# Performance work log

Hardware: AMD Instinct MI355X
Metric: run time of the kernel (lower is better)

The kernel has to match this reference:

```python
import jax, jax.numpy as jnp
import numpy as np

N_NODES = 10000
N_EDGES = 640000
HIDDEN = 128
N_LAYERS = 3
DECAY_RATE = 1.0


def setup_inputs() -> dict:
    key = jax.random.key(0)
    ks = jax.random.split(key, 16)
    D, L = HIDDEN, N_LAYERS
    s = 1.0 / np.sqrt(D)
    inp = {
        "x": jax.random.normal(ks[0], (N_NODES, D), dtype=jnp.float32),
        "edge_index": jax.random.randint(ks[1], (2, N_EDGES), 0, N_NODES, dtype=jnp.int32),
        "confidences": jax.random.uniform(ks[2], (N_NODES,), dtype=jnp.float32),
        # per-layer message MLP params, stacked over layers: [L, D, D] / [L, D]
        "msg_W1": jax.random.normal(ks[3], (L, D, D), dtype=jnp.float32) * s,
        "msg_b1": jnp.zeros((L, D), dtype=jnp.float32),
        "msg_W2": jax.random.normal(ks[4], (L, D, D), dtype=jnp.float32) * s,
        "msg_b2": jnp.zeros((L, D), dtype=jnp.float32),
        # per-layer self MLP params
        "self_W1": jax.random.normal(ks[5], (L, D, D), dtype=jnp.float32) * s,
        "self_b1": jnp.zeros((L, D), dtype=jnp.float32),
        "self_W2": jax.random.normal(ks[6], (L, D, D), dtype=jnp.float32) * s,
        "self_b2": jnp.zeros((L, D), dtype=jnp.float32),
        # layer-importance score net: Linear(D,D) -> ReLU -> Linear(D,1)
        "score_W1": jax.random.normal(ks[7], (D, D), dtype=jnp.float32) * s,
        "score_b1": jnp.zeros((D,), dtype=jnp.float32),
        "score_W2": jax.random.normal(ks[8], (D, 1), dtype=jnp.float32) * s,
        "score_b2": jnp.zeros((1,), dtype=jnp.float32),
    }
    return inp


def _mlp2(h, W1, b1, W2, b2):
    return jax.nn.relu(h @ W1 + b1) @ W2 + b2


def reference(x, edge_index, confidences,
              msg_W1, msg_b1, msg_W2, msg_b2,
              self_W1, self_b1, self_W2, self_b2,
              score_W1, score_b1, score_W2, score_b2):
    src, dst = edge_index[0], edge_index[1]
    # confidence-weighted edge weights: exp(-decay * |c_src - c_dst|)
    edge_weights = jnp.exp(-DECAY_RATE * jnp.abs(confidences[src] - confidences[dst]))  # [E]

    h = x
    layer_outputs = []
    for i in range(N_LAYERS):
        messages = _mlp2(h[src], msg_W1[i], msg_b1[i], msg_W2[i], msg_b2[i])  # [E, D]
        messages = messages * edge_weights[:, None]
        aggr = jax.ops.segment_sum(messages, dst, num_segments=N_NODES)  # [N, D]
        self_loop = _mlp2(h, self_W1[i], self_b1[i], self_W2[i], self_b2[i])
        h = jax.nn.relu(aggr + self_loop)  # dropout is identity in eval mode
        layer_outputs.append(h)

    stacked = jnp.stack(layer_outputs, axis=0)  # [L, N, D]
    scores = _mlp2(stacked, score_W1, score_b1, score_W2, score_b2)[..., 0]  # [L, N]
    layer_weights = jax.nn.softmax(scores, axis=0)  # softmax over layers
    output = jnp.sum(layer_weights[:, :, None] * stacked, axis=0)  # [N, D]
    return output, stacked, layer_weights
```

## Files before the change

kernel.cpp:

```cpp
#include <hip/hip_runtime.h>

#define NN 10000
#define NE 640000
#define D 128
#define NF (NN * D)
#define WS 136
#define WBYTES (D * WS * 2)
#define WCHUNKS (WBYTES / 1024)
#define NBLK 100
#define EPB (NE / NBLK)
#define MPAD 1000000
#define NIT 4
#define GBP 79
#define NCS ((NN + 127) / 128)
#define MZB ((MPAD / 2 + 1023) / 1024)

typedef __bf16 bf16x8 __attribute__((ext_vector_type(8)));
typedef __bf16 bf16x2 __attribute__((ext_vector_type(2)));
typedef float f32x4 __attribute__((ext_vector_type(4)));

__device__ __forceinline__ void async_copy16(const void* g, void* l) {
    __builtin_amdgcn_global_load_lds(
        (const __attribute__((address_space(1))) unsigned int*)g,
        (__attribute__((address_space(3))) unsigned int*)l, 16, 0, 0);
}


__global__ __launch_bounds__(256) void hist_prep_kernel(
    const int* __restrict__ ei, int* __restrict__ cnt_blk, int* __restrict__ local_rank,
    const float2* __restrict__ x2, bf16x2* __restrict__ xbf,
    const float* __restrict__ mW1, const float* __restrict__ mW2,
    const float* __restrict__ sW1, const float* __restrict__ sW2,
    const float* __restrict__ scW1, __bf16* __restrict__ wt,
    float4* __restrict__ metaz) {
    __shared__ unsigned int hist[NN / 2];
    int b = blockIdx.x, t = threadIdx.x;
    if (b < NBLK) {
        for (int i = t; i < NN / 2; i += 256) hist[i] = 0u;
        __syncthreads();
        int base = b * EPB;
#pragma unroll 1
        for (int i = 0; i < EPB / 256; i++) {
            int e = base + i * 256 + t;
            int d = ei[NE + e];
            int sh = (d & 1) * 16;
            unsigned int old = atomicAdd(&hist[d >> 1], 1u << sh);
            local_rank[e] = (old >> sh) & 0xFFFFu;
        }
        __syncthreads();
        for (int i = t; i < NN; i += 256)
            cnt_blk[b * NN + i] = (hist[i >> 1] >> ((i & 1) * 16)) & 0xFFFFu;
    } else if (b < NBLK + 2500) {
        int i = (b - NBLK) * 256 + t;
        float2 v = x2[i];
        bf16x2 o;
        o.x = (__bf16)v.x;
        o.y = (__bf16)v.y;
        xbf[i] = o;
    } else if (b < NBLK + 2513) {
        int m = b - (NBLK + 2500);
        const float* W = (m < 3)   ? mW1 + (size_t)m * D * D
                       : (m < 6)   ? mW2 + (size_t)(m - 3) * D * D
                       : (m < 9)   ? sW1 + (size_t)(m - 6) * D * D
                       : (m < 12)  ? sW2 + (size_t)(m - 9) * D * D
                                   : scW1;
        __bf16* o = wt + (size_t)m * D * WS;
        for (int i = t; i < D * D; i += 256) {
            int k = i >> 7, n = i & 127;
            o[n * WS + k] = (__bf16)W[i];
        }
    } else {
        int base = (b - (NBLK + 2513)) * 1024 + t;
#pragma unroll
        for (int i = 0; i < 4; i++) {
            int idx = base + i * 256;
            if (idx < MPAD / 2) metaz[idx] = make_float4(0.f, 0.f, 0.f, 0.f);
        }
    }
}

__global__ void scan_kernel(const int* __restrict__ cnt, int* __restrict__ row_ptr) {
    __shared__ int lds[256];
    int t = threadIdx.x;
    const int CH = (NN + 255) / 256;
    int base = t * CH;
    int s = 0;
    for (int i = 0; i < CH; i++) {
        int idx = base + i;
        if (idx < NN) s += (cnt[idx] + 31) & ~31;
    }
    lds[t] = s;
    __syncthreads();
    for (int off = 1; off < 256; off <<= 1) {
        int v = (t >= off) ? lds[t - off] : 0;
        __syncthreads();
        lds[t] += v;
        __syncthreads();
    }
    int run = (t == 0) ? 0 : lds[t - 1];
    for (int i = 0; i < CH; i++) {
        int idx = base + i;
        if (idx < NN) {
            row_ptr[idx] = run;
            run += (cnt[idx] + 31) & ~31;
        }
    }
    if (t == 255) row_ptr[NN] = lds[255];
}

__global__ void scatter_kernel(const int* __restrict__ ei, const float* __restrict__ conf,
                               const int* __restrict__ local_rank,
                               const int* __restrict__ cnt_blk,
                               const int* __restrict__ row_ptr, float2* __restrict__ meta) {
    int e = blockIdx.x * 256 + threadIdx.x;
    if (e >= NE) return;
    int s = ei[e];
    int d = ei[NE + e];
    int blk = e / EPB;
    int pos = row_ptr[d] + cnt_blk[blk * NN + d] + local_rank[e];
    meta[pos] = make_float2(__int_as_float(s), expf(-fabsf(conf[s] - conf[d])));
}


__device__ __forceinline__ void mlp_tiles_body(
    const __bf16* __restrict__ Abf,
    const __bf16* __restrict__ Wt1, const float* __restrict__ b1,
    const __bf16* __restrict__ Wt2, const float* __restrict__ b2,
    __bf16* __restrict__ Mbf, float* __restrict__ Cself, int write_bf,
    __bf16 (*Wl)[D * WS], __bf16 (*Tl)[16 * WS], int bx, int t) {
    int wid = t >> 6, lane = t & 63;
    int m16 = lane & 15, q = lane >> 4;

    for (int c = wid; c < 2 * WCHUNKS; c += 2) {
        const char* src = (c < WCHUNKS) ? (const char*)Wt1 + c * 1024
                                        : (const char*)Wt2 + (c - WCHUNKS) * 1024;
        async_copy16(src + lane * 16, (char*)&Wl[0][0] + c * 1024 + lane * 16);
    }

    int rowb = bx * (NIT * 32) + wid * 16;

    bf16x8 af[4];
    {
        int arow = min(rowb + m16, NN - 1);
#pragma unroll
        for (int kk = 0; kk < 4; kk++)
            af[kk] = *(const bf16x8*)&Abf[(size_t)arow * D + kk * 32 + q * 8];
    }
    float b1v[8], b2v[8];
#pragma unroll
    for (int ct = 0; ct < 8; ct++) { b1v[ct] = b1[ct * 16 + m16]; b2v[ct] = b2[ct * 16 + m16]; }

    __syncthreads();

#pragma unroll
    for (int it = 0; it < NIT; it++) {
        int row0 = rowb + it * 32;
        bf16x8 afn[4];
        if (it + 1 < NIT) {
            int arown = min(row0 + 32 + m16, NN - 1);
#pragma unroll
            for (int kk = 0; kk < 4; kk++)
                afn[kk] = *(const bf16x8*)&Abf[(size_t)arown * D + kk * 32 + q * 8];
        }

        f32x4 acc[8];
#pragma unroll
        for (int ct = 0; ct < 8; ct++) acc[ct] = (f32x4){0.f, 0.f, 0.f, 0.f};
#pragma unroll
        for (int kk = 0; kk < 4; kk++) {
#pragma unroll
            for (int ct = 0; ct < 8; ct++) {
                bf16x8 bb = *(const bf16x8*)&Wl[0][(ct * 16 + m16) * WS + kk * 32 + q * 8];
                acc[ct] = __builtin_amdgcn_mfma_f32_16x16x32_bf16(af[kk], bb, acc[ct], 0, 0, 0);
            }
        }
#pragma unroll
        for (int ct = 0; ct < 8; ct++) {
#pragma unroll
            for (int r = 0; r < 4; r++) {
                float v = fmaxf(acc[ct][r] + b1v[ct], 0.f);
                Tl[wid][(q * 4 + r) * WS + ct * 16 + m16] = (__bf16)v;
            }
        }

#pragma unroll
        for (int ct = 0; ct < 8; ct++) acc[ct] = (f32x4){0.f, 0.f, 0.f, 0.f};
#pragma unroll
        for (int kk = 0; kk < 4; kk++) {
            bf16x8 a = *(const bf16x8*)&Tl[wid][m16 * WS + kk * 32 + q * 8];
#pragma unroll
            for (int ct = 0; ct < 8; ct++) {
                bf16x8 bb = *(const bf16x8*)&Wl[1][(ct * 16 + m16) * WS + kk * 32 + q * 8];
                acc[ct] = __builtin_amdgcn_mfma_f32_16x16x32_bf16(a, bb, acc[ct], 0, 0, 0);
            }
        }
        if (write_bf) {
#pragma unroll
            for (int ct = 0; ct < 8; ct++) {
#pragma unroll
                for (int r = 0; r < 4; r++) {
                    int row = row0 + q * 4 + r;
                    if (row < NN) Mbf[(size_t)row * D + ct * 16 + m16] = (__bf16)(acc[ct][r] + b2v[ct]);
                }
            }
        } else {
#pragma unroll
            for (int ct = 0; ct < 8; ct++) {
#pragma unroll
                for (int r = 0; r < 4; r++) {
                    int row = row0 + q * 4 + r;
                    if (row < NN) Cself[(size_t)row * D + ct * 16 + m16] = acc[ct][r] + b2v[ct];
                }
            }
        }
        if (it + 1 < NIT) {
#pragma unroll
            for (int kk = 0; kk < 4; kk++) af[kk] = afn[kk];
        }
    }
}


__global__ __launch_bounds__(128) void mlp_pair_mfma(
    const __bf16* __restrict__ Abf,
    const __bf16* __restrict__ Wt1a, const float* __restrict__ b1a,
    const __bf16* __restrict__ Wt2a, const float* __restrict__ b2a, __bf16* __restrict__ Mbf,
    const __bf16* __restrict__ Wt1b, const float* __restrict__ b1b,
    const __bf16* __restrict__ Wt2b, const float* __restrict__ b2b, float* __restrict__ Cself) {
    __shared__ __align__(16) __bf16 Wl[2][D * WS];
    __shared__ __align__(16) __bf16 Tl[2][16 * WS];
    int pb = blockIdx.y;
    mlp_tiles_body(Abf,
                   pb ? Wt1b : Wt1a, pb ? b1b : b1a,
                   pb ? Wt2b : Wt2a, pb ? b2b : b2a,
                   Mbf, Cself, pb == 0, Wl, Tl, blockIdx.x, threadIdx.x);
}


__global__ __launch_bounds__(128) void mlp0_colsum_kernel(
    const __bf16* __restrict__ Abf,
    const __bf16* __restrict__ Wt1a, const float* __restrict__ b1a,
    const __bf16* __restrict__ Wt2a, const float* __restrict__ b2a, __bf16* __restrict__ Mbf,
    const __bf16* __restrict__ Wt1b, const float* __restrict__ b1b,
    const __bf16* __restrict__ Wt2b, const float* __restrict__ b2b, float* __restrict__ Cself,
    int* __restrict__ cnt_blk, int* __restrict__ cnt) {
    __shared__ __align__(16) __bf16 Wl[2][D * WS];
    __shared__ __align__(16) __bf16 Tl[2][16 * WS];
    int b = blockIdx.x, t = threadIdx.x;

    if (b < NCS) {
        int n = b * 128 + t;
        if (n >= NN) return;
        int acc = 0;
#pragma unroll
        for (int g = 0; g < 4; g++) {
            int v[25];
#pragma unroll
            for (int k = 0; k < 25; k++) v[k] = cnt_blk[(g * 25 + k) * NN + n];
#pragma unroll
            for (int k = 0; k < 25; k++) {
                cnt_blk[(g * 25 + k) * NN + n] = acc;
                acc += v[k];
            }
        }
        cnt[n] = acc;
        return;
    }

    int mb = b - NCS;
    int pb = (mb >= GBP);
    int bx = pb ? mb - GBP : mb;
    mlp_tiles_body(Abf,
                   pb ? Wt1b : Wt1a, pb ? b1b : b1a,
                   pb ? Wt2b : Wt2a, pb ? b2b : b2a,
                   Mbf, Cself, pb == 0, Wl, Tl, bx, t);
}


__global__ __launch_bounds__(256) void aggregate_kernel(
    const uint4* __restrict__ Mbf4, const float4* __restrict__ Mself4,
    const int* __restrict__ row_ptr, const float2* __restrict__ meta,
    float4* __restrict__ out4, bf16x8* __restrict__ stbf8) {
    int wid = (blockIdx.x * 256 + threadIdx.x) >> 6;
    int lane = threadIdx.x & 63;
    int q = lane >> 4, l4 = lane & 15, l5 = lane & 31;
    int beg = row_ptr[wid], end = row_ptr[wid + 1];
    float a[8] = {0.f, 0.f, 0.f, 0.f, 0.f, 0.f, 0.f, 0.f};
    float2 mcur = meta[beg + l5];
    for (int j = beg; j < end; j += 32) {
        float2 mnext = meta[j + 32 + l5];
        int srcid[8];
        float wgt[8];
#pragma unroll
        for (int u = 0; u < 8; u++) {
            int sl = 4 * u + q;
            srcid[u] = __float_as_int(__shfl(mcur.x, sl));
            wgt[u] = __shfl(mcur.y, sl);
        }
        uint4 g[8];
#pragma unroll
        for (int u = 0; u < 8; u++) g[u] = Mbf4[(size_t)srcid[u] * 16 + l4];
#pragma unroll
        for (int u = 0; u < 8; u++) {
            float w = wgt[u];
            a[0] = fmaf(w, __uint_as_float(g[u].x << 16), a[0]);
            a[1] = fmaf(w, __uint_as_float(g[u].x & 0xFFFF0000u), a[1]);
            a[2] = fmaf(w, __uint_as_float(g[u].y << 16), a[2]);
            a[3] = fmaf(w, __uint_as_float(g[u].y & 0xFFFF0000u), a[3]);
            a[4] = fmaf(w, __uint_as_float(g[u].z << 16), a[4]);
            a[5] = fmaf(w, __uint_as_float(g[u].z & 0xFFFF0000u), a[5]);
            a[6] = fmaf(w, __uint_as_float(g[u].w << 16), a[6]);
            a[7] = fmaf(w, __uint_as_float(g[u].w & 0xFFFF0000u), a[7]);
        }
        mcur = mnext;
    }
#pragma unroll
    for (int i = 0; i < 8; i++) {
        a[i] += __shfl_xor(a[i], 16);
        a[i] += __shfl_xor(a[i], 32);
    }
    if (q == 0) {
        float4 sv0 = Mself4[(size_t)wid * 32 + 2 * l4];
        float4 sv1 = Mself4[(size_t)wid * 32 + 2 * l4 + 1];
        float4 r0, r1;
        r0.x = fmaxf(a[0] + sv0.x, 0.f);
        r0.y = fmaxf(a[1] + sv0.y, 0.f);
        r0.z = fmaxf(a[2] + sv0.z, 0.f);
        r0.w = fmaxf(a[3] + sv0.w, 0.f);
        r1.x = fmaxf(a[4] + sv1.x, 0.f);
        r1.y = fmaxf(a[5] + sv1.y, 0.f);
        r1.z = fmaxf(a[6] + sv1.z, 0.f);
        r1.w = fmaxf(a[7] + sv1.w, 0.f);
        out4[(size_t)wid * 32 + 2 * l4] = r0;
        out4[(size_t)wid * 32 + 2 * l4 + 1] = r1;
        bf16x8 hb;
        hb[0] = (__bf16)r0.x; hb[1] = (__bf16)r0.y;
        hb[2] = (__bf16)r0.z; hb[3] = (__bf16)r0.w;
        hb[4] = (__bf16)r1.x; hb[5] = (__bf16)r1.y;
        hb[6] = (__bf16)r1.z; hb[7] = (__bf16)r1.w;
        stbf8[(size_t)wid * 16 + l4] = hb;
    }
}


__global__ __launch_bounds__(256) void score_finalize_mfma(
    const __bf16* __restrict__ stbf, const float* __restrict__ st,
    const __bf16* __restrict__ Wt1, const float* __restrict__ b1,
    const float* __restrict__ w2, const float* __restrict__ b2,
    float* __restrict__ out, float* __restrict__ lw_out) {
    __shared__ __align__(16) __bf16 Wl[D * WS];
    __shared__ float sc_l[3][64];
    __shared__ float lw_l[3][64];
    int t = threadIdx.x;
    int wid = t >> 6, lane = t & 63;
    int m16 = lane & 15, q = lane >> 4;
    int row0 = blockIdx.x * 64;

    for (int c = wid; c < WCHUNKS; c += 4)
        async_copy16((const char*)Wt1 + c * 1024 + lane * 16,
                     (char*)&Wl[0] + c * 1024 + lane * 16);
    __syncthreads();

    int arow = min(row0 + wid * 16 + m16, NN - 1);
    float bb = b2[0];

    for (int l = 0; l < 3; l++) {
        const __bf16* A = stbf + (size_t)l * NF;
        f32x4 acc[8];
#pragma unroll
        for (int ct = 0; ct < 8; ct++) acc[ct] = (f32x4){0.f, 0.f, 0.f, 0.f};
#pragma unroll
        for (int kk = 0; kk < 4; kk++) {
            bf16x8 a = *(const bf16x8*)&A[(size_t)arow * D + kk * 32 + q * 8];
#pragma unroll
            for (int ct = 0; ct < 8; ct++) {
                bf16x8 b = *(const bf16x8*)&Wl[(ct * 16 + m16) * WS + kk * 32 + q * 8];
                acc[ct] = __builtin_amdgcn_mfma_f32_16x16x32_bf16(a, b, acc[ct], 0, 0, 0);
            }
        }
        float p[4] = {0.f, 0.f, 0.f, 0.f};
#pragma unroll
        for (int ct = 0; ct < 8; ct++) {
            float bv = b1[ct * 16 + m16];
            float wv = w2[ct * 16 + m16];
#pragma unroll
            for (int r = 0; r < 4; r++) p[r] += fmaxf(acc[ct][r] + bv, 0.f) * wv;
        }
#pragma unroll
        for (int r = 0; r < 4; r++) {
#pragma unroll
            for (int off = 1; off < 16; off <<= 1) p[r] += __shfl_xor(p[r], off);
            if (m16 == 0) sc_l[l][wid * 16 + q * 4 + r] = p[r] + bb;
        }
    }
    __syncthreads();

    if (t < 64) {
        int row = row0 + t;
        float s0 = sc_l[0][t], s1 = sc_l[1][t], s2 = sc_l[2][t];
        float m = fmaxf(s0, fmaxf(s1, s2));
        float e0 = expf(s0 - m), e1 = expf(s1 - m), e2 = expf(s2 - m);
        float inv = 1.f / (e0 + e1 + e2);
        lw_l[0][t] = e0 * inv;
        lw_l[1][t] = e1 * inv;
        lw_l[2][t] = e2 * inv;
        if (row < NN) {
            lw_out[row] = e0 * inv;
            lw_out[NN + row] = e1 * inv;
            lw_out[2 * NN + row] = e2 * inv;
        }
    }
    __syncthreads();

    for (int i = t; i < 64 * 32; i += 256) {
        int r = i >> 5, c4 = i & 31;
        int row = row0 + r;
        if (row >= NN) break;
        float4 v0 = ((const float4*)(st + (size_t)row * D))[c4];
        float4 v1 = ((const float4*)(st + (size_t)NF + (size_t)row * D))[c4];
        float4 v2 = ((const float4*)(st + 2 * (size_t)NF + (size_t)row * D))[c4];
        float w0 = lw_l[0][r], w1 = lw_l[1][r], w2v = lw_l[2][r];
        float4 o;
        o.x = w0 * v0.x + w1 * v1.x + w2v * v2.x;
        o.y = w0 * v0.y + w1 * v1.y + w2v * v2.y;
        o.z = w0 * v0.z + w1 * v1.z + w2v * v2.z;
        o.w = w0 * v0.w + w1 * v1.w + w2v * v2.w;
        ((float4*)(out + (size_t)row * D))[c4] = o;
    }
}

extern "C" void kernel_launch(void* const* d_in, const int* in_sizes, int n_in,
                              void* d_out, int out_size, void* d_ws, size_t ws_size,
                              hipStream_t stream) {
    const float* x = (const float*)d_in[0];
    const int* ei = (const int*)d_in[1];
    const float* conf = (const float*)d_in[2];
    const float* msg_W1 = (const float*)d_in[3];
    const float* msg_b1 = (const float*)d_in[4];
    const float* msg_W2 = (const float*)d_in[5];
    const float* msg_b2 = (const float*)d_in[6];
    const float* self_W1 = (const float*)d_in[7];
    const float* self_b1 = (const float*)d_in[8];
    const float* self_W2 = (const float*)d_in[9];
    const float* self_b2 = (const float*)d_in[10];
    const float* score_W1 = (const float*)d_in[11];
    const float* score_b1 = (const float*)d_in[12];
    const float* score_W2 = (const float*)d_in[13];
    const float* score_b2 = (const float*)d_in[14];

    float* out = (float*)d_out;
    float* out_stacked = out + NF;
    float* out_lw = out + 4 * (size_t)NF;

    float* w = (float*)d_ws;
    float* Mself = w;
    float2* meta = (float2*)(w + (size_t)NF);
    __bf16* xbf = (__bf16*)(meta + MPAD);
    __bf16* stbf = xbf + (size_t)NF;
    __bf16* Mbf = stbf + 3 * (size_t)NF;
    __bf16* wt = Mbf + (size_t)NF;
    int* local_rank = (int*)(wt + 13 * (size_t)D * WS);
    int* cnt_blk = local_rank + NE;
    int* row_ptr = cnt_blk + NBLK * NN;
    int* cnt = row_ptr + NN + 1;

    const size_t MAT = (size_t)D * WS;
    const int GE = (NE + 255) / 256;
    const int GB64 = (NN + 63) / 64;

    hist_prep_kernel<<<NBLK + 2513 + MZB, 256, 0, stream>>>(
        ei, cnt_blk, local_rank, (const float2*)x, (bf16x2*)xbf,
        msg_W1, msg_W2, self_W1, self_W2, score_W1, wt,
        (float4*)meta);
    mlp0_colsum_kernel<<<NCS + 2 * GBP, 128, 0, stream>>>(
        xbf,
        wt + 0 * MAT, msg_b1, wt + 3 * MAT, msg_b2, Mbf,
        wt + 6 * MAT, self_b1, wt + 9 * MAT, self_b2, Mself,
        cnt_blk, cnt);
    scan_kernel<<<1, 256, 0, stream>>>(cnt, row_ptr);
    scatter_kernel<<<GE, 256, 0, stream>>>(ei, conf, local_rank, cnt_blk, row_ptr, meta);
    aggregate_kernel<<<NN / 4, 256, 0, stream>>>(
        (const uint4*)Mbf, (const float4*)Mself, row_ptr, meta,
        (float4*)(out_stacked + 0 * (size_t)NF), (bf16x8*)(stbf + 0 * (size_t)NF));

    for (int l = 1; l < 3; l++) {
        const __bf16* a_in = stbf + (size_t)(l - 1) * NF;
        mlp_pair_mfma<<<dim3(GBP, 2), 128, 0, stream>>>(
            a_in,
            wt + (size_t)l * MAT, msg_b1 + (size_t)l * D,
            wt + (size_t)(3 + l) * MAT, msg_b2 + (size_t)l * D, Mbf,
            wt + (size_t)(6 + l) * MAT, self_b1 + (size_t)l * D,
            wt + (size_t)(9 + l) * MAT, self_b2 + (size_t)l * D, Mself);
        aggregate_kernel<<<NN / 4, 256, 0, stream>>>(
            (const uint4*)Mbf, (const float4*)Mself, row_ptr, meta,
            (float4*)(out_stacked + (size_t)l * NF),
            (bf16x8*)(stbf + (size_t)l * NF));
    }

    score_finalize_mfma<<<GB64, 256, 0, stream>>>(
        stbf, out_stacked, wt + 12 * MAT, score_b1, score_W2, score_b2, out, out_lw);
}
```

Measured before the change: 248.3 us.

## Read MLP weights directly from global memory instead of staging in LDS

Drops the async global-to-LDS staging of the bf16 weight matrices in the MLP and score kernels, and reads the B operands straight from global memory (cached in L1/L2). The MLP kernels change from 128-thread blocks looping over 4 row tiles to 256-thread blocks processing 64 rows each with no inner loop, which doubles the grid. The aim is to cut LDS footprint and the barrier at the start of each block, raising occupancy. In exchange, every wave refetches weights through the vector memory path, which may add cache traffic and latency on the MFMA operand loads.

Result: no change. 245.7 us (-1.1%).

```diff
diff --git a/kernel.cpp b/kernel.cpp
--- a/kernel.cpp
+++ b/kernel.cpp
@@ -5,25 +5,17 @@
 #define D 128
 #define NF (NN * D)
 #define WS 136
-#define WBYTES (D * WS * 2)
-#define WCHUNKS (WBYTES / 1024)
 #define NBLK 100
 #define EPB (NE / NBLK)
 #define MPAD 1000000
-#define NIT 4
-#define GBP 79
-#define NCS ((NN + 127) / 128)
 #define MZB ((MPAD / 2 + 1023) / 1024)
+#define NCS2 ((NN + 255) / 256)
+#define GMB 157
+#define GE ((NE + 255) / 256)
 
 typedef __bf16 bf16x8 __attribute__((ext_vector_type(8)));
 typedef __bf16 bf16x2 __attribute__((ext_vector_type(2)));
 typedef float f32x4 __attribute__((ext_vector_type(4)));
-
-__device__ __forceinline__ void async_copy16(const void* g, void* l) {
-    __builtin_amdgcn_global_load_lds(
-        (const __attribute__((address_space(1))) unsigned int*)g,
-        (__attribute__((address_space(3))) unsigned int*)l, 16, 0, 0);
-}
 
 
 __global__ __launch_bounds__(256) void hist_prep_kernel(
@@ -122,158 +114,126 @@
 }
 
 
-__device__ __forceinline__ void mlp_tiles_body(
+__device__ __forceinline__ void mlp_nostage_body(
     const __bf16* __restrict__ Abf,
     const __bf16* __restrict__ Wt1, const float* __restrict__ b1,
     const __bf16* __restrict__ Wt2, const float* __restrict__ b2,
     __bf16* __restrict__ Mbf, float* __restrict__ Cself, int write_bf,
-    __bf16 (*Wl)[D * WS], __bf16 (*Tl)[16 * WS], int bx, int t) {
+    __bf16 (*Tl)[16 * WS], int bx, int t) {
     int wid = t >> 6, lane = t & 63;
     int m16 = lane & 15, q = lane >> 4;
-
-    for (int c = wid; c < 2 * WCHUNKS; c += 2) {
-        const char* src = (c < WCHUNKS) ? (const char*)Wt1 + c * 1024
-                                        : (const char*)Wt2 + (c - WCHUNKS) * 1024;
-        async_copy16(src + lane * 16, (char*)&Wl[0][0] + c * 1024 + lane * 16);
-    }
-
-    int rowb = bx * (NIT * 32) + wid * 16;
+    int row0 = bx * 64 + wid * 16;
+    int arow = min(row0 + m16, NN - 1);
 
     bf16x8 af[4];
-    {
-        int arow = min(rowb + m16, NN - 1);
-#pragma unroll
-        for (int kk = 0; kk < 4; kk++)
-            af[kk] = *(const bf16x8*)&Abf[(size_t)arow * D + kk * 32 + q * 8];
-    }
+#pragma unroll
+    for (int kk = 0; kk < 4; kk++)
+        af[kk] = *(const bf16x8*)&Abf[(size_t)arow * D + kk * 32 + q * 8];
     float b1v[8], b2v[8];
 #pragma unroll
     for (int ct = 0; ct < 8; ct++) { b1v[ct] = b1[ct * 16 + m16]; b2v[ct] = b2[ct * 16 + m16]; }
 
-    __syncthreads();
-
-#pragma unroll
-    for (int it = 0; it < NIT; it++) {
-        int row0 = rowb + it * 32;
-        bf16x8 afn[4];
-        if (it + 1 < NIT) {
-            int arown = min(row0 + 32 + m16, NN - 1);
-#pragma unroll
-            for (int kk = 0; kk < 4; kk++)
-                afn[kk] = *(const bf16x8*)&Abf[(size_t)arown * D + kk * 32 + q * 8];
-        }
-
-        f32x4 acc[8];
-#pragma unroll
-        for (int ct = 0; ct < 8; ct++) acc[ct] = (f32x4){0.f, 0.f, 0.f, 0.f};
-#pragma unroll
-        for (int kk = 0; kk < 4; kk++) {
-#pragma unroll
-            for (int ct = 0; ct < 8; ct++) {
-                bf16x8 bb = *(const bf16x8*)&Wl[0][(ct * 16 + m16) * WS + kk * 32 + q * 8];
-                acc[ct] = __builtin_amdgcn_mfma_f32_16x16x32_bf16(af[kk], bb, acc[ct], 0, 0, 0);
+    f32x4 acc[8];
+#pragma unroll
+    for (int ct = 0; ct < 8; ct++) acc[ct] = (f32x4){0.f, 0.f, 0.f, 0.f};
+#pragma unroll
+    for (int kk = 0; kk < 4; kk++) {
+#pragma unroll
+        for (int ct = 0; ct < 8; ct++) {
+            bf16x8 bb = *(const bf16x8*)&Wt1[(ct * 16 + m16) * WS + kk * 32 + q * 8];
+            acc[ct] = __builtin_amdgcn_mfma_f32_16x16x32_bf16(af[kk], bb, acc[ct], 0, 0, 0);
+        }
+    }
+#pragma unroll
+    for (int ct = 0; ct < 8; ct++) {
+#pragma unroll
+        for (int r = 0; r < 4; r++) {
+            float v = fmaxf(acc[ct][r] + b1v[ct], 0.f);
+            Tl[wid][(q * 4 + r) * WS + ct * 16 + m16] = (__bf16)v;
+        }
+    }
+
+#pragma unroll
+    for (int ct = 0; ct < 8; ct++) acc[ct] = (f32x4){0.f, 0.f, 0.f, 0.f};
+#pragma unroll
+    for (int kk = 0; kk < 4; kk++) {
+        bf16x8 a = *(const bf16x8*)&Tl[wid][m16 * WS + kk * 32 + q * 8];
+#pragma unroll
+        for (int ct = 0; ct < 8; ct++) {
+            bf16x8 bb = *(const bf16x8*)&Wt2[(ct * 16 + m16) * WS + kk * 32 + q * 8];
+            acc[ct] = __builtin_amdgcn_mfma_f32_16x16x32_bf16(a, bb, acc[ct], 0, 0, 0);
+        }
+    }
+    if (write_bf) {
+#pragma unroll
+        for (int ct = 0; ct < 8; ct++) {
+#pragma unroll
+            for (int r = 0; r < 4; r++) {
+                int row = row0 + q * 4 + r;
+                if (row < NN) Mbf[(size_t)row * D + ct * 16 + m16] = (__bf16)(acc[ct][r] + b2v[ct]);
             }
         }
+    } else {
 #pragma unroll
         for (int ct = 0; ct < 8; ct++) {
 #pragma unroll
             for (int r = 0; r < 4; r++) {
-                float v = fmaxf(acc[ct][r] + b1v[ct], 0.f);
-                Tl[wid][(q * 4 + r) * WS + ct * 16 + m16] = (__bf16)v;
+                int row = row0 + q * 4 + r;
+                if (row < NN) Cself[(size_t)row * D + ct * 16 + m16] = acc[ct][r] + b2v[ct];
             }
         }
-
-#pragma unroll
-        for (int ct = 0; ct < 8; ct++) acc[ct] = (f32x4){0.f, 0.f, 0.f, 0.f};
-#pragma unroll
-        for (int kk = 0; kk < 4; kk++) {
-            bf16x8 a = *(const bf16x8*)&Tl[wid][m16 * WS + kk * 32 + q * 8];
-#pragma unroll
-            for (int ct = 0; ct < 8; ct++) {
-                bf16x8 bb = *(const bf16x8*)&Wl[1][(ct * 16 + m16) * WS + kk * 32 + q * 8];
-                acc[ct] = __builtin_amdgcn_mfma_f32_16x16x32_bf16(a, bb, acc[ct], 0, 0, 0);
+    }
+}
+
+
+__global__ __launch_bounds__(256) void mlp0_colsum_kernel(
+    const __bf16* __restrict__ Abf,
+    const __bf16* __restrict__ Wt1m, const float* __restrict__ b1m,
+    const __bf16* __restrict__ Wt2m, const float* __restrict__ b2m, __bf16* __restrict__ Mbf,
+    const __bf16* __restrict__ Wt1s, const float* __restrict__ b1s,
+    const __bf16* __restrict__ Wt2s, const float* __restrict__ b2s, float* __restrict__ Cself,
+    int* __restrict__ cnt_blk, int* __restrict__ cnt) {
+    __shared__ __align__(16) __bf16 Tl[4][16 * WS];
+    int b = blockIdx.x, t = threadIdx.x;
+
+    if (b < NCS2) {
+        int n = b * 256 + t;
+        if (n >= NN) return;
+        int acc = 0;
+#pragma unroll
+        for (int g = 0; g < 4; g++) {
+            int v[25];
+#pragma unroll
+            for (int k = 0; k < 25; k++) v[k] = cnt_blk[(g * 25 + k) * NN + n];
+#pragma unroll
+            for (int k = 0; k < 25; k++) {
+                cnt_blk[(g * 25 + k) * NN + n] = acc;
+                acc += v[k];
             }
         }
-        if (write_bf) {
-#pragma unroll
-            for (int ct = 0; ct < 8; ct++) {
-#pragma unroll
-                for (int r = 0; r < 4; r++) {
-                    int row = row0 + q * 4 + r;
-                    if (row < NN) Mbf[(size_t)row * D + ct * 16 + m16] = (__bf16)(acc[ct][r] + b2v[ct]);
-                }
-            }
-        } else {
-#pragma unroll
-            for (int ct = 0; ct < 8; ct++) {
-#pragma unroll
-                for (int r = 0; r < 4; r++) {
-                    int row = row0 + q * 4 + r;
-                    if (row < NN) Cself[(size_t)row * D + ct * 16 + m16] = acc[ct][r] + b2v[ct];
-                }
-            }
-        }
-        if (it + 1 < NIT) {
-#pragma unroll
-            for (int kk = 0; kk < 4; kk++) af[kk] = afn[kk];
-        }
-    }
-}
-
-
-__global__ __launch_bounds__(128) void mlp_pair_mfma(
+        cnt[n] = acc;
+        return;
+    }
+    int mb = b - NCS2;
+    if (mb < GMB)
+        mlp_nostage_body(Abf, Wt1m, b1m, Wt2m, b2m, Mbf, nullptr, 1, Tl, mb, t);
+    else
+        mlp_nostage_body(Abf, Wt1s, b1s, Wt2s, b2s, nullptr, Cself, 0, Tl, mb - GMB, t);
+}
+
+
+__global__ __launch_bounds__(256) void mlp_pair_mfma(
     const __bf16* __restrict__ Abf,
     const __bf16* __restrict__ Wt1a, const float* __restrict__ b1a,
     const __bf16* __restrict__ Wt2a, const float* __restrict__ b2a, __bf16* __restrict__ Mbf,
     const __bf16* __restrict__ Wt1b, const float* __restrict__ b1b,
     const __bf16* __restrict__ Wt2b, const float* __restrict__ b2b, float* __restrict__ Cself) {
-    __shared__ __align__(16) __bf16 Wl[2][D * WS];
-    __shared__ __align__(16) __bf16 Tl[2][16 * WS];
+    __shared__ __align__(16) __bf16 Tl[4][16 * WS];
     int pb = blockIdx.y;
-    mlp_tiles_body(Abf,
-                   pb ? Wt1b : Wt1a, pb ? b1b : b1a,
-                   pb ? Wt2b : Wt2a, pb ? b2b : b2a,
-                   Mbf, Cself, pb == 0, Wl, Tl, blockIdx.x, threadIdx.x);
-}
-
-
-__global__ __launch_bounds__(128) void mlp0_colsum_kernel(
-    const __bf16* __restrict__ Abf,
-    const __bf16* __restrict__ Wt1a, const float* __restrict__ b1a,
-    const __bf16* __restrict__ Wt2a, const float* __restrict__ b2a, __bf16* __restrict__ Mbf,
-    const __bf16* __restrict__ Wt1b, const float* __restrict__ b1b,
-    const __bf16* __restrict__ Wt2b, const float* __restrict__ b2b, float* __restrict__ Cself,
-    int* __restrict__ cnt_blk, int* __restrict__ cnt) {
-    __shared__ __align__(16) __bf16 Wl[2][D * WS];
-    __shared__ __align__(16) __bf16 Tl[2][16 * WS];
-    int b = blockIdx.x, t = threadIdx.x;
-
-    if (b < NCS) {
-        int n = b * 128 + t;
-        if (n >= NN) return;
-        int acc = 0;
-#pragma unroll
-        for (int g = 0; g < 4; g++) {
-            int v[25];
-#pragma unroll
-            for (int k = 0; k < 25; k++) v[k] = cnt_blk[(g * 25 + k) * NN + n];
-#pragma unroll
-            for (int k = 0; k < 25; k++) {
-                cnt_blk[(g * 25 + k) * NN + n] = acc;
-                acc += v[k];
-            }
-        }
-        cnt[n] = acc;
-        return;
-    }
-
-    int mb = b - NCS;
-    int pb = (mb >= GBP);
-    int bx = pb ? mb - GBP : mb;
-    mlp_tiles_body(Abf,
-                   pb ? Wt1b : Wt1a, pb ? b1b : b1a,
-                   pb ? Wt2b : Wt2a, pb ? b2b : b2a,
-                   Mbf, Cself, pb == 0, Wl, Tl, bx, t);
+    mlp_nostage_body(Abf,
+                     pb ? Wt1b : Wt1a, pb ? b1b : b1a,
+                     pb ? Wt2b : Wt2a, pb ? b2b : b2a,
+                     Mbf, Cself, pb == 0, Tl, blockIdx.x, threadIdx.x);
 }
 
 
@@ -348,7 +308,6 @@
     const __bf16* __restrict__ Wt1, const float* __restrict__ b1,
     const float* __restrict__ w2, const float* __restrict__ b2,
     float* __restrict__ out, float* __restrict__ lw_out) {
-    __shared__ __align__(16) __bf16 Wl[D * WS];
     __shared__ float sc_l[3][64];
     __shared__ float lw_l[3][64];
     int t = threadIdx.x;
@@ -356,11 +315,6 @@
     int m16 = lane & 15, q = lane >> 4;
     int row0 = blockIdx.x * 64;
 
-    for (int c = wid; c < WCHUNKS; c += 4)
-        async_copy16((const char*)Wt1 + c * 1024 + lane * 16,
-                     (char*)&Wl[0] + c * 1024 + lane * 16);
-    __syncthreads();
-
     int arow = min(row0 + wid * 16 + m16, NN - 1);
     float bb = b2[0];
 
@@ -374,7 +328,7 @@
             bf16x8 a = *(const bf16x8*)&A[(size_t)arow * D + kk * 32 + q * 8];
 #pragma unroll
             for (int ct = 0; ct < 8; ct++) {
-                bf16x8 b = *(const bf16x8*)&Wl[(ct * 16 + m16) * WS + kk * 32 + q * 8];
+                bf16x8 b = *(const bf16x8*)&Wt1[(ct * 16 + m16) * WS + kk * 32 + q * 8];
                 acc[ct] = __builtin_amdgcn_mfma_f32_16x16x32_bf16(a, b, acc[ct], 0, 0, 0);
             }
         }
@@ -465,14 +419,13 @@
     int* cnt = row_ptr + NN + 1;
 
     const size_t MAT = (size_t)D * WS;
-    const int GE = (NE + 255) / 256;
     const int GB64 = (NN + 63) / 64;
 
     hist_prep_kernel<<<NBLK + 2513 + MZB, 256, 0, stream>>>(
         ei, cnt_blk, local_rank, (const float2*)x, (bf16x2*)xbf,
         msg_W1, msg_W2, self_W1, self_W2, score_W1, wt,
         (float4*)meta);
-    mlp0_colsum_kernel<<<NCS + 2 * GBP, 128, 0, stream>>>(
+    mlp0_colsum_kernel<<<NCS2 + 2 * GMB, 256, 0, stream>>>(
         xbf,
         wt + 0 * MAT, msg_b1, wt + 3 * MAT, msg_b2, Mbf,
         wt + 6 * MAT, self_b1, wt + 9 * MAT, self_b2, Mself,
@@ -485,7 +438,7 @@
 
     for (int l = 1; l < 3; l++) {
         const __bf16* a_in = stbf + (size_t)(l - 1) * NF;
-        mlp_pair_mfma<<<dim3(GBP, 2), 128, 0, stream>>>(
+        mlp_pair_mfma<<<dim3(GMB, 2), 256, 0, stream>>>(
             a_in,
             wt + (size_t)l * MAT, msg_b1 + (size_t)l * D,
             wt + (size_t)(3 + l) * MAT, msg_b2 + (size_t)l * D, Mbf,
```
